# Performance work log

Hardware: AMD Instinct MI355X
Metric: run time of the kernel (lower is better)

## Reference

```python
import jax, jax.numpy as jnp
import numpy as np

KS = 7
STRIDE = 2
C = 96


def _parabolic_kernel(t):
    # z_i = linspace(-ks//2 + 1, ks//2, ks) -> symmetric offsets for odd ks
    z = jnp.linspace(-(KS // 2) + 1 - 1 + 1, KS // 2, KS, dtype=jnp.float32)  # == linspace(-ks//2+1, ks//2, ks)
    z = jnp.linspace(float(-(KS // 2) + 1), float(KS // 2), KS, dtype=jnp.float32)
    z2 = z[:, None] ** 2 + z[None, :] ** 2            # [ks, ks]
    return -z2[None, :, :] / (4.0 * t[:, None, None])  # [C, ks, ks]


def setup_inputs() -> dict:
    key = jax.random.key(0)
    k1, k2 = jax.random.split(key)
    f = jax.random.normal(k1, (16, C, 224, 224), dtype=jnp.float32)
    t = jax.random.uniform(k2, (C,), dtype=jnp.float32, minval=0.25, maxval=4.0)
    return {"f": f, "t": t}


def reference(f, t):
    # Morphological dilation (max-plus pooling) with per-channel parabolic kernel.
    h = _parabolic_kernel(t)  # [C, ks, ks]
    B, Cc, H, W = f.shape
    pad = KS // 2
    Ho = (H + 2 * pad - KS) // STRIDE + 1
    Wo = (W + 2 * pad - KS) // STRIDE + 1
    neg_inf = jnp.float32(-jnp.inf)
    fp = jnp.pad(f, ((0, 0), (0, 0), (pad, pad), (pad, pad)), constant_values=neg_inf)
    out = jnp.full((B, Cc, Ho, Wo), neg_inf, dtype=f.dtype)
    for ki in range(KS):
        for kj in range(KS):
            win = jax.lax.slice(
                fp,
                (0, 0, ki, kj),
                (B, Cc, ki + (Ho - 1) * STRIDE + 1, kj + (Wo - 1) * STRIDE + 1),
                (1, 1, STRIDE, STRIDE),
            )  # [B, C, Ho, Wo]
            out = jnp.maximum(out, win + h[:, ki, kj][None, :, None, None])
    return out
```

## Files before the change

### kernel.cpp

```cpp
#include <hip/hip_runtime.h>
#include <math.h>


#define KS     7
#define C_CH   96
#define B_SZ   16
#define H_IN   224
#define W_IN   224
#define H_OUT  112
#define W_OUT  112
#define TW     4
#define TH     16
#define KX     (W_OUT / TW)
#define KYV    (H_OUT / TH)
#define NROWS  (2 * TH + 5)

__global__ __launch_bounds__(256, 4)
void parab_pool2d_kernel(const float* __restrict__ f,
                         const float* __restrict__ t,
                         float* __restrict__ out)
{
    const int idx = blockIdx.x * 256 + threadIdx.x;
    const int k   = idx % KX;
    const int tyv = (idx / KX) % KYV;
    const int c   = (idx / (KX * KYV)) % C_CH;
    const int b   =  idx / (KX * KYV * C_CH);

    const float s = 1.0f / (4.0f * t[c]);
    float g[KS];
#pragma unroll
    for (int j = 0; j < KS; ++j) {
        const float z = -2.0f + (float)j * (5.0f / 6.0f);
        g[j] = -(z * z) * s;
    }

    const int wo0     = k * TW;
    const int ho0     = tyv * TH;
    const int colbase = 2 * wo0 - 4;
    const int ibase   = 2 * ho0 - 3;

    const float  NEG = -INFINITY;
    const float4 N4  = make_float4(NEG, NEG, NEG, NEG);

    const float* __restrict__ plane = f + (b * C_CH + c) * (H_IN * W_IN);
    float* __restrict__ obase =
        out + ((b * C_CH + c) * H_OUT + ho0) * W_OUT + wo0;

    const bool kzero = (k == 0);
    const bool klast = (k == KX - 1);
    const int  off0  = kzero ? 4 : 0;
    const int  off3  = klast ? 8 : 12;

    float acc[TH][TW];
#pragma unroll
    for (int d = 0; d < TH; ++d)
#pragma unroll
        for (int m = 0; m < TW; ++m) acc[d][m] = NEG;

#pragma unroll
    for (int r = 0; r < NROWS; ++r) {
        const int  i     = ibase + r;
        const bool rowok = (i >= 0) && (i < H_IN);
        const int  isafe = rowok ? i : 0;
        const float* rb  = plane + isafe * W_IN + colbase;

        float4 a0 = *(const float4*)(rb + off0);
        float4 a1 = *(const float4*)(rb + 4);
        float4 a2 = *(const float4*)(rb + 8);
        float4 a3 = *(const float4*)(rb + off3);
        if (kzero) a0 = N4;
        if (klast) a3 = N4;

        const float v[16] = {a0.x,a0.y,a0.z,a0.w, a1.x,a1.y,a1.z,a1.w,
                             a2.x,a2.y,a2.z,a2.w, a3.x,a3.y,a3.z,a3.w};

        float rm[TW];
#pragma unroll
        for (int m = 0; m < TW; ++m) {
            float x =    v[2*m + 1] + g[0];
            x = fmaxf(x, v[2*m + 2] + g[1]);
            x = fmaxf(x, v[2*m + 3] + g[2]);
            x = fmaxf(x, v[2*m + 4] + g[3]);
            x = fmaxf(x, v[2*m + 5] + g[4]);
            x = fmaxf(x, v[2*m + 6] + g[5]);
            x = fmaxf(x, v[2*m + 7] + g[6]);
            rm[m] = rowok ? x : NEG;
        }

#pragma unroll
        for (int d = 0; d < TH; ++d) {
            if (r >= 2 * d && r <= 2 * d + 6) {
#pragma unroll
                for (int m = 0; m < TW; ++m)
                    acc[d][m] = fmaxf(acc[d][m], rm[m] + g[r - 2 * d]);
            }
        }

        if (r >= 6 && ((r - 6) & 1) == 0) {
            const int d = (r - 6) / 2;
            *(float4*)(obase + d * W_OUT) =
                make_float4(acc[d][0], acc[d][1], acc[d][2], acc[d][3]);
        }
    }
}

extern "C" void kernel_launch(void* const* d_in, const int* in_sizes, int n_in,
                              void* d_out, int out_size, void* d_ws, size_t ws_size,
                              hipStream_t stream) {
    const float* f = (const float*)d_in[0];
    const float* t = (const float*)d_in[1];
    float* out = (float*)d_out;

    const int total   = B_SZ * C_CH * KYV * KX;
    const int threads = 256;
    const int blocks  = total / threads;
    parab_pool2d_kernel<<<blocks, threads, 0, stream>>>(f, t, out);
}
```

Baseline: 96.55 us.

## Map one wavefront per row strip and share halo columns via lane shuffles

Each wavefront now covers a full 112-column output strip of 16 rows. Each of its 56 active lanes loads one float4 per input row and gets its horizontal halo from neighbouring lanes through shuffles, where before each thread made four overlapping float4 loads for 4 output columns. This cuts redundant global loads and makes the row loads fully coalesced. In exchange, 8 of the 64 lanes sit idle, shuffle instructions are added, and the stores shrink to float2. The occupancy hint in launch_bounds is also dropped.

```diff
diff --git a/kernel.cpp b/kernel.cpp
--- a/kernel.cpp
+++ b/kernel.cpp
@@ -9,22 +9,23 @@
 #define W_IN   224
 #define H_OUT  112
 #define W_OUT  112
-#define TW     4
 #define TH     16
-#define KX     (W_OUT / TW)
 #define KYV    (H_OUT / TH)
 #define NROWS  (2 * TH + 5)
+#define NWAVES (B_SZ * C_CH * KYV)
 
-__global__ __launch_bounds__(256, 4)
+__global__ __launch_bounds__(256)
 void parab_pool2d_kernel(const float* __restrict__ f,
                          const float* __restrict__ t,
                          float* __restrict__ out)
 {
-    const int idx = blockIdx.x * 256 + threadIdx.x;
-    const int k   = idx % KX;
-    const int tyv = (idx / KX) % KYV;
-    const int c   = (idx / (KX * KYV)) % C_CH;
-    const int b   =  idx / (KX * KYV * C_CH);
+    const int lane = threadIdx.x & 63;
+    const int wave = blockIdx.x * 4 + (threadIdx.x >> 6);
+
+    const int tyv  = wave % KYV;
+    const int rest = wave / KYV;
+    const int c    = rest % C_CH;
+    const int b    = rest / C_CH;
 
     const float s = 1.0f / (4.0f * t[c]);
     float g[KS];
@@ -34,72 +35,67 @@
         g[j] = -(z * z) * s;
     }
 
-    const int wo0     = k * TW;
-    const int ho0     = tyv * TH;
-    const int colbase = 2 * wo0 - 4;
-    const int ibase   = 2 * ho0 - 3;
+    const int ho0   = tyv * TH;
+    const int ibase = 2 * ho0 - 3;
 
-    const float  NEG = -INFINITY;
-    const float4 N4  = make_float4(NEG, NEG, NEG, NEG);
+    const bool active = (lane < 56);
+    const bool l0     = (lane == 0);
+    const bool l55    = (lane == 55);
+    const int  colL   = active ? 4 * lane : 220;
 
+    const float NEG = -INFINITY;
     const float* __restrict__ plane = f + (b * C_CH + c) * (H_IN * W_IN);
     float* __restrict__ obase =
-        out + ((b * C_CH + c) * H_OUT + ho0) * W_OUT + wo0;
+        out + ((b * C_CH + c) * H_OUT + ho0) * W_OUT + 2 * lane;
 
-    const bool kzero = (k == 0);
-    const bool klast = (k == KX - 1);
-    const int  off0  = kzero ? 4 : 0;
-    const int  off3  = klast ? 8 : 12;
-
-    float acc[TH][TW];
+    float acc[TH][2];
 #pragma unroll
-    for (int d = 0; d < TH; ++d)
-#pragma unroll
-        for (int m = 0; m < TW; ++m) acc[d][m] = NEG;
+    for (int d = 0; d < TH; ++d) { acc[d][0] = NEG; acc[d][1] = NEG; }
 
 #pragma unroll
     for (int r = 0; r < NROWS; ++r) {
         const int  i     = ibase + r;
         const bool rowok = (i >= 0) && (i < H_IN);
         const int  isafe = rowok ? i : 0;
-        const float* rb  = plane + isafe * W_IN + colbase;
 
-        float4 a0 = *(const float4*)(rb + off0);
-        float4 a1 = *(const float4*)(rb + 4);
-        float4 a2 = *(const float4*)(rb + 8);
-        float4 a3 = *(const float4*)(rb + off3);
-        if (kzero) a0 = N4;
-        if (klast) a3 = N4;
+        const float4 o = *(const float4*)(plane + isafe * W_IN + colL);
 
-        const float v[16] = {a0.x,a0.y,a0.z,a0.w, a1.x,a1.y,a1.z,a1.w,
-                             a2.x,a2.y,a2.z,a2.w, a3.x,a3.y,a3.z,a3.w};
+        float ly = __shfl_up(o.y, 1);
+        float lz = __shfl_up(o.z, 1);
+        float lw = __shfl_up(o.w, 1);
+        float rx = __shfl_down(o.x, 1);
+        float ry = __shfl_down(o.y, 1);
+        if (l0)  { ly = NEG; lz = NEG; lw = NEG; }
+        if (l55) { rx = NEG; ry = NEG; }
 
-        float rm[TW];
-#pragma unroll
-        for (int m = 0; m < TW; ++m) {
-            float x =    v[2*m + 1] + g[0];
-            x = fmaxf(x, v[2*m + 2] + g[1]);
-            x = fmaxf(x, v[2*m + 3] + g[2]);
-            x = fmaxf(x, v[2*m + 4] + g[3]);
-            x = fmaxf(x, v[2*m + 5] + g[4]);
-            x = fmaxf(x, v[2*m + 6] + g[5]);
-            x = fmaxf(x, v[2*m + 7] + g[6]);
-            rm[m] = rowok ? x : NEG;
-        }
+        float rm0 =        ly  + g[0];
+        rm0 = fmaxf(rm0,   lz  + g[1]);
+        rm0 = fmaxf(rm0,   lw  + g[2]);
+        rm0 = fmaxf(rm0,   o.x + g[3]);
+        rm0 = fmaxf(rm0,   o.y + g[4]);
+        rm0 = fmaxf(rm0,   o.z + g[5]);
+        rm0 = fmaxf(rm0,   o.w + g[6]);
+        float rm1 =        lw  + g[0];
+        rm1 = fmaxf(rm1,   o.x + g[1]);
+        rm1 = fmaxf(rm1,   o.y + g[2]);
+        rm1 = fmaxf(rm1,   o.z + g[3]);
+        rm1 = fmaxf(rm1,   o.w + g[4]);
+        rm1 = fmaxf(rm1,   rx  + g[5]);
+        rm1 = fmaxf(rm1,   ry  + g[6]);
+        if (!rowok) { rm0 = NEG; rm1 = NEG; }
 
 #pragma unroll
         for (int d = 0; d < TH; ++d) {
             if (r >= 2 * d && r <= 2 * d + 6) {
-#pragma unroll
-                for (int m = 0; m < TW; ++m)
-                    acc[d][m] = fmaxf(acc[d][m], rm[m] + g[r - 2 * d]);
+                acc[d][0] = fmaxf(acc[d][0], rm0 + g[r - 2 * d]);
+                acc[d][1] = fmaxf(acc[d][1], rm1 + g[r - 2 * d]);
             }
         }
 
         if (r >= 6 && ((r - 6) & 1) == 0) {
             const int d = (r - 6) / 2;
-            *(float4*)(obase + d * W_OUT) =
-                make_float4(acc[d][0], acc[d][1], acc[d][2], acc[d][3]);
+            if (active)
+                *(float2*)(obase + d * W_OUT) = make_float2(acc[d][0], acc[d][1]);
         }
     }
 }
@@ -111,8 +107,7 @@
     const float* t = (const float*)d_in[1];
     float* out = (float*)d_out;
 
-    const int total   = B_SZ * C_CH * KYV * KX;
     const int threads = 256;
-    const int blocks  = total / threads;
+    const int blocks  = NWAVES / 4;
     parab_pool2d_kernel<<<blocks, threads, 0, stream>>>(f, t, out);
 }
```

After: 80.16 us. -17.0%, faster.
